# Kernel tuning notes

Measured on AMD Instinct MI355X. Metric: run time of the kernel, lower is better.

The kernel has to match this reference:

```python
import jax, jax.numpy as jnp
import numpy as np
from jax import lax

K_SIZE = 3
STRIDE = 1
PADDING = 1


def setup_inputs() -> dict:
    key = jax.random.key(0)
    k1, k2, k3 = jax.random.split(key, 3)
    x = jax.random.normal(k1, (4, 64, 64, 256), dtype=jnp.float32)
    # small offsets so bilinear sampling stays near the regular grid (realistic DCN behavior)
    offset_w = jax.random.normal(k2, (3, 3, 256, 27), dtype=jnp.float32) * 0.01
    offset_b = jnp.zeros((1, 1, 1, 27), dtype=jnp.float32)
    dcn_weight = jax.random.normal(k3, (256, 256, 3, 3), dtype=jnp.float32) * 0.02
    return {"x": x, "offset_w": offset_w, "offset_b": offset_b, "dcn_weight": dcn_weight}


def _dcnv2(x, offset_w, offset_b, dcn_weight):
    k, stride, padding = K_SIZE, STRIDE, PADDING
    N, H, W, C = x.shape
    kk = k * k
    # offset/mask prediction conv (stride=1 -> SAME padding, per original code)
    om = lax.conv_general_dilated(
        x, offset_w, window_strides=(stride, stride), padding='SAME',
        dimension_numbers=('NHWC', 'HWIO', 'NHWC')) + offset_b
    offset = om[..., : 2 * kk]                      # [N,oH,oW,2k^2] (y,x) pairs
    mask = jax.nn.sigmoid(om[..., 2 * kk:])         # [N,oH,oW,k^2]
    oH = (H + 2 * padding - (k - 1)) // stride
    oW = (W + 2 * padding - (k - 1)) // stride
    # asymmetric zero padding ((p, p+1), (p, p+1)) as in the original
    pad_x = jnp.pad(x, ((0, 0), (padding, padding + 1), (padding, padding + 1), (0, 0)))
    # sampling grid: base center + fixed kernel offsets + learned offsets
    base_y = jnp.arange(oH, dtype=x.dtype) * stride + padding   # [oH]
    base_x = jnp.arange(oW, dtype=x.dtype) * stride + padding   # [oW]
    kr = jnp.arange(k, dtype=x.dtype) - (k - 1) / 2.0
    inner_y = jnp.repeat(kr, k)   # [k^2], row-major (kH, kW)
    inner_x = jnp.tile(kr, k)
    off_yx = offset.reshape(N, oH, oW, kk, 2)
    pos_y = base_y[None, :, None, None] + inner_y[None, None, None, :] + off_yx[..., 0]
    pos_x = base_x[None, None, :, None] + inner_x[None, None, None, :] + off_yx[..., 1]
    pos_y = jnp.clip(pos_y, 0.0, H + 2 * padding - 1.0)
    pos_x = jnp.clip(pos_x, 0.0, W + 2 * padding - 1.0)
    y1 = jnp.floor(pos_y)
    x1 = jnp.floor(pos_x)
    y1i = y1.astype(jnp.int32)
    x1i = x1.astype(jnp.int32)
    y2i = y1i + 1
    x2i = x1i + 1
    gather = jax.vmap(lambda px, yi, xi: px[yi, xi])  # per-sample [oH,oW,k^2] -> [oH,oW,k^2,C]
    v1 = gather(pad_x, y1i, x1i)
    v2 = gather(pad_x, y1i, x2i)
    v3 = gather(pad_x, y2i, x1i)
    v4 = gather(pad_x, y2i, x2i)
    lh = (pos_y - y1)[..., None]
    lw = (pos_x - x1)[..., None]
    hh = 1.0 - lh
    hw = 1.0 - lw
    value = (hh * hw * v1 + hh * lw * v2 + lh * hw * v3 + lh * lw * v4) * mask[..., None]
    # [N,oH,oW,k^2,C] -> [N,oH,oW,C,k^2] -> [N,oH,oW,C*k^2], matching original layout
    value = jnp.transpose(value, (0, 1, 2, 4, 3)).reshape(N, oH, oW, C * kk)
    w = jnp.transpose(dcn_weight, (1, 2, 3, 0)).reshape(C * kk, -1)  # [C*k^2, out_C]
    return jnp.einsum('nhwc,cf->nhwf', value, w)


def reference(x, offset_w, offset_b, dcn_weight):
    return _dcnv2(x, offset_w, offset_b, dcn_weight)
```

## Files before the change

kernel.cpp:

```cpp
#include <hip/hip_runtime.h>
#include <hip/hip_fp16.h>
#include <math.h>

typedef __attribute__((ext_vector_type(8))) _Float16 f16x8;
typedef __attribute__((ext_vector_type(4))) float f32x4;

#define XP_OFF   0
#define XP_BYTES (4*67*67*256*2)
#define WT_OFF   XP_BYTES
#define WT_BYTES (2304*256*2)
#define WOT_OFF  (WT_OFF + WT_BYTES)
#define WOT_BYTES (2304*32*2)
#define OM_OFF   (WOT_OFF + WOT_BYTES)
#define OM_BYTES (16384*32*4)
#define V_OFF    (OM_OFF + OM_BYTES)
#define V_BYTES  ((size_t)16384*2304*2)
#define WS_NEED  ((size_t)V_OFF + V_BYTES)

#define AS1(p) ((const __attribute__((address_space(1))) void*)(p))
#define AS3(p) ((__attribute__((address_space(3))) void*)(p))

__global__ __launch_bounds__(256) void prep_all(const float* __restrict__ x,
        const float* __restrict__ dw, const float* __restrict__ ow,
        __half* __restrict__ xp, __half* __restrict__ wt, __half* __restrict__ wot) {
    int b = blockIdx.x, tid = threadIdx.x;
    if (b < 2245) {
        int g = b * 256 + tid;
        if (g >= 17956 * 32) return;
        int row = g >> 5, sub = g & 31;
        int n = row / 4489, rem = row - n * 4489;
        int yy = rem / 67,  xx = rem - yy * 67;
        __half* dst = xp + (size_t)row * 256 + sub * 8;
        union { uint4 u; __half2 h[4]; } r;
        r.u = make_uint4(0u, 0u, 0u, 0u);
        if (yy >= 1 && yy <= 64 && xx >= 1 && xx <= 64) {
            const float* src = x + (((size_t)n * 64 + (yy - 1)) * 64 + (xx - 1)) * 256 + sub * 8;
            float4 a = *(const float4*)src;
            float4 c = *(const float4*)(src + 4);
            r.h[0] = __float22half2_rn(make_float2(a.x, a.y));
            r.h[1] = __float22half2_rn(make_float2(a.z, a.w));
            r.h[2] = __float22half2_rn(make_float2(c.x, c.y));
            r.h[3] = __float22half2_rn(make_float2(c.z, c.w));
        }
        *(uint4*)dst = r.u;
    } else if (b < 2501) {
        int oc = b - 2245, c = tid;
        const float* src = dw + oc * 2304 + c * 9;
        __half* dst = wt + oc * 2304 + c;
        #pragma unroll
        for (int t = 0; t < 9; ++t) dst[t * 256] = __float2half(src[t]);
    } else {
        int g = (b - 2501) * 256 + tid;
        int oc = g & 31, idx = g >> 5;
        float v = (oc < 27) ? ow[idx * 27 + oc] : 0.f;
        wot[oc * 2304 + idx] = __float2half(v);
    }
}

__global__ __launch_bounds__(256) void offset_mfma4(const __half* __restrict__ xp,
        const __half* __restrict__ wot, const float* __restrict__ ob,
        float* __restrict__ om) {
    __shared__ __align__(16) char sA[2][16384];
    int tid = threadIdx.x, lane = tid & 63, wave = tid >> 6;
    int bid = blockIdx.x;
    int mt = (bid & 7) * 64 + (bid >> 3);
    int p0 = mt * 32;
    int n = p0 >> 12, y = (p0 & 4095) >> 6, w0 = p0 & 63;
    const char* xpn = (const char*)(xp + (size_t)n * 4489 * 256);
    int wr = wave >> 1, wc = wave & 1;
    int ar = lane & 15, kl = (lane >> 4) * 8;

    int soff[4];
    #pragma unroll
    for (int q = 0; q < 4; ++q) {
        int d = (q * 256 + tid) * 16;
        int row = d >> 9;
        soff[q] = row * 512 + ((d & 511) ^ ((row & 7) << 4));
    }

    f32x4 acc = {0.f, 0.f, 0.f, 0.f};
    int r_a = wr * 16 + ar;
    int rsw = (r_a & 7) << 4;
    const __half* bb = wot + (size_t)(wc * 16 + ar) * 2304 + kl;

    #pragma unroll
    for (int q = 0; q < 4; ++q)
        __builtin_amdgcn_global_load_lds(AS1(xpn + ((y * 67 + w0) << 9) + soff[q]),
                                         AS3(&sA[0][(q * 256 + tid) * 16]), 16, 0, 0);
    __syncthreads();

    for (int t = 0; t < 9; ++t) {
        int buf = t & 1;
        if (t < 8) {
            int t1 = t + 1;
            int ty = t1 / 3, tx = t1 - 3 * ty;
            int sb = ((y + ty) * 67 + w0 + tx) << 9;
            #pragma unroll
            for (int q = 0; q < 4; ++q)
                __builtin_amdgcn_global_load_lds(AS1(xpn + sb + soff[q]),
                                                 AS3(&sA[buf ^ 1][(q * 256 + tid) * 16]), 16, 0, 0);
        }
        const __half* bp = bb + t * 256;
        #pragma unroll
        for (int c0 = 0; c0 < 256; c0 += 32) {
            f16x8 a = *(const f16x8*)(&sA[buf][0] + r_a * 512 + (((c0 + kl) * 2) ^ rsw));
            f16x8 b = *(const f16x8*)(bp + c0);
            acc = __builtin_amdgcn_mfma_f32_16x16x32_f16(a, b, acc, 0, 0, 0);
        }
        __syncthreads();
    }

    int col = wc * 16 + ar;
    float bias = (col < 27) ? ob[col] : 0.f;
    int rj = (lane >> 4) * 4;
    #pragma unroll
    for (int j = 0; j < 4; ++j)
        om[(size_t)(p0 + wr * 16 + rj + j) * 32 + col] = acc[j] + bias;
}

__global__ __launch_bounds__(256) void sample_v(const __half* __restrict__ xp,
        const float* __restrict__ om, __half* __restrict__ V) {
    int g = blockIdx.x * 256 + threadIdx.x;
    int j = g >> 5;
    int s = g & 31;
    int p = j / 9;
    int t = j - p * 9;
    int n = p >> 12, y = (p >> 6) & 63, w = p & 63;
    const float* omp = om + (size_t)p * 32;
    float offy = omp[2 * t];
    float offx = omp[2 * t + 1];
    float mraw = omp[18 + t];
    float mask = 1.f / (1.f + __expf(-mraw));
    float py = (float)(y + 1) + (float)(t / 3 - 1) + offy;
    float px = (float)(w + 1) + (float)(t % 3 - 1) + offx;
    py = fminf(fmaxf(py, 0.f), 65.f);
    px = fminf(fmaxf(px, 0.f), 65.f);
    float y1f = floorf(py), x1f = floorf(px);
    int y1 = (int)y1f, x1 = (int)x1f;
    float ly = py - y1f, lx = px - x1f, hy = 1.f - ly, hx = 1.f - lx;
    const __half* b = xp + (size_t)n * 4489 * 256 + ((y1 * 67 + x1) << 8) + s * 8;
    union { uint4 u; __half2 h[4]; } cA, cB, cC, cD, r;
    cA.u = *(const uint4*)(b);
    cB.u = *(const uint4*)(b + 256);
    cC.u = *(const uint4*)(b + 17152);
    cD.u = *(const uint4*)(b + 17408);
    __half2 W11 = __float2half2_rn(hy * hx * mask), W12 = __float2half2_rn(hy * lx * mask);
    __half2 W21 = __float2half2_rn(ly * hx * mask), W22 = __float2half2_rn(ly * lx * mask);
    #pragma unroll
    for (int i = 0; i < 4; ++i)
        r.h[i] = __hfma2(cD.h[i], W22, __hfma2(cC.h[i], W21,
                 __hfma2(cB.h[i], W12, __hmul2(cA.h[i], W11))));
    *(uint4*)((char*)V + (size_t)g * 16) = r.u;
}

__global__ __launch_bounds__(256) void gemm_v2(const __half* __restrict__ V,
        const __half* __restrict__ wt, float* __restrict__ out) {
    __shared__ __align__(16) char sA[2][8192];
    __shared__ __align__(16) char sB[2][16384];
    int tid = threadIdx.x, lane = tid & 63, wave = tid >> 6;
    int bid = blockIdx.x;
    int xcd = bid & 7, idx = bid >> 3;
    int mt = xcd * 32 + (idx >> 1);
    int nt = idx & 1;
    int p0 = mt * 64, oc0 = nt * 128;
    int wr = wave >> 1, wc = wave & 1;
    int ar = lane & 15, kl = (lane >> 4) * 8;

    const char* aS[2]; const char* bS[4];
    #pragma unroll
    for (int q = 0; q < 2; ++q) {
        int d = (q * 256 + tid) * 16;
        int row = d >> 7, wb = d & 127;
        aS[q] = (const char*)V + (size_t)(p0 + row) * 4608 + (wb ^ ((row & 7) << 4));
    }
    #pragma unroll
    for (int q = 0; q < 4; ++q) {
        int d = (q * 256 + tid) * 16;
        int row = d >> 7, wb = d & 127;
        bS[q] = (const char*)wt + (size_t)(oc0 + row) * 4608 + (wb ^ ((row & 7) << 4));
    }

    f32x4 acc[2][4];
    #pragma unroll
    for (int m = 0; m < 2; ++m)
        #pragma unroll
        for (int nn = 0; nn < 4; ++nn) acc[m][nn] = (f32x4){0.f,0.f,0.f,0.f};

    #pragma unroll
    for (int q = 0; q < 2; ++q)
        __builtin_amdgcn_global_load_lds(AS1(aS[q]), AS3(&sA[0][(q * 256 + tid) * 16]), 16, 0, 0);
    #pragma unroll
    for (int q = 0; q < 4; ++q)
        __builtin_amdgcn_global_load_lds(AS1(bS[q]), AS3(&sB[0][(q * 256 + tid) * 16]), 16, 0, 0);
    __syncthreads();

    for (int kt = 0; kt < 36; ++kt) {
        int buf = kt & 1;
        if (kt < 35) {
            int kb = (kt + 1) * 128;
            #pragma unroll
            for (int q = 0; q < 2; ++q)
                __builtin_amdgcn_global_load_lds(AS1(aS[q] + kb), AS3(&sA[buf ^ 1][(q * 256 + tid) * 16]), 16, 0, 0);
            #pragma unroll
            for (int q = 0; q < 4; ++q)
                __builtin_amdgcn_global_load_lds(AS1(bS[q] + kb), AS3(&sB[buf ^ 1][(q * 256 + tid) * 16]), 16, 0, 0);
        }
        #pragma unroll
        for (int kk = 0; kk < 2; ++kk) {
            int ko = kk * 64 + kl * 2;
            f16x8 af[2], bf[4];
            #pragma unroll
            for (int m = 0; m < 2; ++m) {
                int r = wr * 32 + m * 16 + ar;
                af[m] = *(const f16x8*)(&sA[buf][0] + r * 128 + (ko ^ ((r & 7) << 4)));
            }
            #pragma unroll
            for (int nn = 0; nn < 4; ++nn) {
                int r = wc * 64 + nn * 16 + ar;
                bf[nn] = *(const f16x8*)(&sB[buf][0] + r * 128 + (ko ^ ((r & 7) << 4)));
            }
            #pragma unroll
            for (int m = 0; m < 2; ++m)
                #pragma unroll
                for (int nn = 0; nn < 4; ++nn)
                    acc[m][nn] = __builtin_amdgcn_mfma_f32_16x16x32_f16(af[m], bf[nn], acc[m][nn], 0, 0, 0);
        }
        __syncthreads();
    }

    int rj = (lane >> 4) * 4;
    #pragma unroll
    for (int m = 0; m < 2; ++m)
        #pragma unroll
        for (int nn = 0; nn < 4; ++nn)
            #pragma unroll
            for (int j = 0; j < 4; ++j)
                out[(size_t)(p0 + wr * 32 + m * 16 + rj + j) * 256 + oc0 + wc * 64 + nn * 16 + ar] = acc[m][nn][j];
}

__global__ __launch_bounds__(512) void dcn_mfma3(const __half* __restrict__ xp,
        const float* __restrict__ om, const __half* __restrict__ wt,
        float* __restrict__ out) {
    __shared__ char  s_v[16 * 512];
    __shared__ float s_ly[16][9], s_lx[16][9], s_m[16][9];
    __shared__ int   s_y1[16][9], s_x1[16][9];
    int tid  = threadIdx.x;
    int lane = tid & 63;
    int wave = tid >> 6;
    int bid  = blockIdx.x;
    int swzb = (bid & 7) * 128 + (bid >> 3);
    int p0 = swzb * 16;
    int n  = p0 >> 12;
    int y  = (p0 & 4095) >> 6;
    int w0 = p0 & 63;
    const __half* xpn = xp + (size_t)n * 4489 * 256;
    if (tid < 144) {
        int ps = tid / 9, k = tid - 9 * ps;
        int p  = p0 + ps;
        float offy = om[(size_t)p * 32 + 2 * k];
        float offx = om[(size_t)p * 32 + 2 * k + 1];
        float mraw = om[(size_t)p * 32 + 18 + k];
        float mask = 1.f / (1.f + __expf(-mraw));
        float py = (float)(y + 1)       + (float)(k / 3 - 1) + offy;
        float px = (float)(w0 + ps + 1) + (float)(k % 3 - 1) + offx;
        py = fminf(fmaxf(py, 0.f), 65.f);
        px = fminf(fmaxf(px, 0.f), 65.f);
        float y1f = floorf(py), x1f = floorf(px);
        s_y1[ps][k] = (int)y1f;
        s_x1[ps][k] = (int)x1f;
        s_ly[ps][k] = py - y1f;
        s_lx[ps][k] = px - x1f;
        s_m [ps][k] = mask;
    }
    __syncthreads();
    int px = tid >> 5;
    int ch = (tid & 31) * 8;
    int ar = lane & 15;
    int kl = (lane >> 4) * 8;
    int oc0 = wave * 32;
    const __half* bp0 = wt + (size_t)(oc0 + ar) * 2304 + kl;
    const __half* bp1 = wt + (size_t)(oc0 + 16 + ar) * 2304 + kl;
    int wr_off = px * 512 + (((tid & 31) * 16) ^ ((px & 7) << 4));
    int rd_row = ar * 512;
    int rd_swz = (ar & 7) << 4;
    f32x4 acc0 = {0.f,0.f,0.f,0.f}, acc1 = {0.f,0.f,0.f,0.f};
    for (int t = 0; t < 9; ++t) {
        int y1 = s_y1[px][t], x1 = s_x1[px][t];
        const __half* b = xpn + ((size_t)(y1 * 67 + x1) << 8) + ch;
        union { uint4 u; __half2 h[4]; } cA, cB, cC, cD, r;
        cA.u = *(const uint4*)(b);
        cB.u = *(const uint4*)(b + 256);
        cC.u = *(const uint4*)(b + 17152);
        cD.u = *(const uint4*)(b + 17408);
        float ly = s_ly[px][t], lx = s_lx[px][t], mk = s_m[px][t];
        float hy = 1.f - ly, hx = 1.f - lx;
        __half2 W11 = __float2half2_rn(hy * hx * mk);
        __half2 W12 = __float2half2_rn(hy * lx * mk);
        __half2 W21 = __float2half2_rn(ly * hx * mk);
        __half2 W22 = __float2half2_rn(ly * lx * mk);
        #pragma unroll
        for (int i = 0; i < 4; ++i)
            r.h[i] = __hfma2(cD.h[i], W22, __hfma2(cC.h[i], W21,
                     __hfma2(cB.h[i], W12, __hmul2(cA.h[i], W11))));
        *(uint4*)(s_v + wr_off) = r.u;
        __syncthreads();
        const __half* b0 = bp0 + t * 256;
        const __half* b1 = bp1 + t * 256;
        #pragma unroll
        for (int c0 = 0; c0 < 256; c0 += 32) {
            f16x8 a   = *(const f16x8*)(s_v + rd_row + (((c0 + kl) * 2) ^ rd_swz));
            f16x8 vb0 = *(const f16x8*)(b0 + c0);
            f16x8 vb1 = *(const f16x8*)(b1 + c0);
            acc0 = __builtin_amdgcn_mfma_f32_16x16x32_f16(a, vb0, acc0, 0, 0, 0);
            acc1 = __builtin_amdgcn_mfma_f32_16x16x32_f16(a, vb1, acc1, 0, 0, 0);
        }
        __syncthreads();
    }
    int rj = (lane >> 4) * 4;
    #pragma unroll
    for (int j = 0; j < 4; ++j) {
        out[(size_t)(p0 + rj + j) * 256 + oc0 + ar]      = acc0[j];
        out[(size_t)(p0 + rj + j) * 256 + oc0 + 16 + ar] = acc1[j];
    }
}

extern "C" void kernel_launch(void* const* d_in, const int* in_sizes, int n_in,
                              void* d_out, int out_size, void* d_ws, size_t ws_size,
                              hipStream_t stream) {
    const float* x  = (const float*)d_in[0];
    const float* ow = (const float*)d_in[1];
    const float* ob = (const float*)d_in[2];
    const float* dw = (const float*)d_in[3];
    __half* xpp = (__half*)((char*)d_ws + XP_OFF);
    __half* wt  = (__half*)((char*)d_ws + WT_OFF);
    __half* wot = (__half*)((char*)d_ws + WOT_OFF);
    float*  omp = (float*)((char*)d_ws + OM_OFF);
    __half* Vp  = (__half*)((char*)d_ws + V_OFF);
    float* out = (float*)d_out;

    hipLaunchKernelGGL(prep_all,     dim3(2789), dim3(256), 0, stream, x, dw, ow, xpp, wt, wot);
    hipLaunchKernelGGL(offset_mfma4, dim3(512),  dim3(256), 0, stream, xpp, wot, ob, omp);
    if (ws_size >= WS_NEED) {
        hipLaunchKernelGGL(sample_v, dim3(18432), dim3(256), 0, stream, xpp, omp, Vp);
        hipLaunchKernelGGL(gemm_v2,  dim3(512),   dim3(256), 0, stream, Vp, wt, out);
    } else {
        hipLaunchKernelGGL(dcn_mfma3, dim3(1024), dim3(512), 0, stream, xpp, omp, wt, out);
    }
}
```

Before: 85.11 us.

## Load GEMM B operand from pre-swizzled fragment layout directly into registers

Adds a prep pass that writes the deformable-conv weights in an MFMA-fragment-ordered layout, so the new GEMM kernel loads B fragments straight from global memory into registers instead of staging them through LDS. The GEMM now uses 128-thread blocks where each wave computes a 64x64 tile, with only A double-buffered in LDS and the k-loop manually unrolled by two. The sampling kernel also gets an XCD-aware block remap. This cuts LDS traffic and LDS size per block, in exchange for more registers per thread, fewer waves per block, and reliance on cache hits for the repeated B fragment loads.

```diff
diff --git a/kernel.cpp b/kernel.cpp
--- a/kernel.cpp
+++ b/kernel.cpp
@@ -9,7 +9,9 @@
 #define XP_BYTES (4*67*67*256*2)
 #define WT_OFF   XP_BYTES
 #define WT_BYTES (2304*256*2)
-#define WOT_OFF  (WT_OFF + WT_BYTES)
+#define WTF_OFF  (WT_OFF + WT_BYTES)
+#define WTF_BYTES (2304*256*2)
+#define WOT_OFF  (WTF_OFF + WTF_BYTES)
 #define WOT_BYTES (2304*32*2)
 #define OM_OFF   (WOT_OFF + WOT_BYTES)
 #define OM_BYTES (16384*32*4)
@@ -22,7 +24,8 @@
 
 __global__ __launch_bounds__(256) void prep_all(const float* __restrict__ x,
         const float* __restrict__ dw, const float* __restrict__ ow,
-        __half* __restrict__ xp, __half* __restrict__ wt, __half* __restrict__ wot) {
+        __half* __restrict__ xp, __half* __restrict__ wt, __half* __restrict__ wtf,
+        __half* __restrict__ wot) {
     int b = blockIdx.x, tid = threadIdx.x;
     if (b < 2245) {
         int g = b * 256 + tid;
@@ -49,8 +52,21 @@
         __half* dst = wt + oc * 2304 + c;
         #pragma unroll
         for (int t = 0; t < 9; ++t) dst[t * 256] = __float2half(src[t]);
+    } else if (b < 2789) {
+        int g = (b - 2501) * 256 + tid;
+        int l = g & 63, G = g >> 6;
+        int kg = G % 72, ocg = G / 72;
+        int oc = ocg * 16 + (l & 15);
+        int k  = kg * 32 + ((l >> 4) << 3);
+        int t  = k >> 8, c = k & 255;
+        const float* src = dw + (size_t)oc * 2304 + c * 9 + t;
+        union { uint4 u; __half2 h[4]; } r;
+        #pragma unroll
+        for (int j = 0; j < 4; ++j)
+            r.h[j] = __floats2half2_rn(src[(2 * j) * 9], src[(2 * j + 1) * 9]);
+        *(uint4*)(wtf + (size_t)g * 8) = r.u;
     } else {
-        int g = (b - 2501) * 256 + tid;
+        int g = (b - 2789) * 256 + tid;
         int oc = g & 31, idx = g >> 5;
         float v = (oc < 27) ? ow[idx * 27 + oc] : 0.f;
         wot[oc * 2304 + idx] = __float2half(v);
@@ -104,8 +120,8 @@
         #pragma unroll
         for (int c0 = 0; c0 < 256; c0 += 32) {
             f16x8 a = *(const f16x8*)(&sA[buf][0] + r_a * 512 + (((c0 + kl) * 2) ^ rsw));
-            f16x8 b = *(const f16x8*)(bp + c0);
-            acc = __builtin_amdgcn_mfma_f32_16x16x32_f16(a, b, acc, 0, 0, 0);
+            f16x8 bfr = *(const f16x8*)(bp + c0);
+            acc = __builtin_amdgcn_mfma_f32_16x16x32_f16(a, bfr, acc, 0, 0, 0);
         }
         __syncthreads();
     }
@@ -120,7 +136,9 @@
 
 __global__ __launch_bounds__(256) void sample_v(const __half* __restrict__ xp,
         const float* __restrict__ om, __half* __restrict__ V) {
-    int g = blockIdx.x * 256 + threadIdx.x;
+    int bid = blockIdx.x;
+    int gb  = (bid & 7) * 2304 + (bid >> 3);
+    int g = gb * 256 + threadIdx.x;
     int j = g >> 5;
     int s = g & 31;
     int p = j / 9;
@@ -153,89 +171,88 @@
     *(uint4*)((char*)V + (size_t)g * 16) = r.u;
 }
 
-__global__ __launch_bounds__(256) void gemm_v2(const __half* __restrict__ V,
-        const __half* __restrict__ wt, float* __restrict__ out) {
+#define STAGE_A(DST, KT) do { \
+    _Pragma("unroll") \
+    for (int q = 0; q < 4; ++q) \
+        __builtin_amdgcn_global_load_lds(AS1(aS[q] + (size_t)(KT) * 128), \
+                                         AS3((DST) + (q * 128 + tid) * 16), 16, 0, 0); \
+} while (0)
+
+#define LOAD_B(D0, D1, KT) do { \
+    _Pragma("unroll") \
+    for (int nn = 0; nn < 4; ++nn) { \
+        D0[nn] = *(const f16x8*)(bbase + ((size_t)nn * 72 + (KT) * 2 + 0) * 512); \
+        D1[nn] = *(const f16x8*)(bbase + ((size_t)nn * 72 + (KT) * 2 + 1) * 512); \
+    } \
+} while (0)
+
+#define STEP_K(SBUF, BARR, KK) do { \
+    _Pragma("unroll") \
+    for (int m = 0; m < 4; ++m) { \
+        int r_ = m * 16 + ar; \
+        f16x8 af_ = *(const f16x8*)((SBUF) + r_ * 128 + (((KK) * 64 + kl * 2) ^ ((r_ & 7) << 4))); \
+        _Pragma("unroll") \
+        for (int nn = 0; nn < 4; ++nn) \
+            acc[m][nn] = __builtin_amdgcn_mfma_f32_16x16x32_f16(af_, (BARR)[nn], acc[m][nn], 0, 0, 0); \
+    } \
+} while (0)
+
+__global__ __launch_bounds__(128) void gemm_v3(const __half* __restrict__ V,
+        const __half* __restrict__ wtf, float* __restrict__ out) {
     __shared__ __align__(16) char sA[2][8192];
-    __shared__ __align__(16) char sB[2][16384];
-    int tid = threadIdx.x, lane = tid & 63, wave = tid >> 6;
+    int tid = threadIdx.x, lane = tid & 63, wv = tid >> 6;
     int bid = blockIdx.x;
     int xcd = bid & 7, idx = bid >> 3;
     int mt = xcd * 32 + (idx >> 1);
     int nt = idx & 1;
-    int p0 = mt * 64, oc0 = nt * 128;
-    int wr = wave >> 1, wc = wave & 1;
+    int p0 = mt * 64;
     int ar = lane & 15, kl = (lane >> 4) * 8;
 
-    const char* aS[2]; const char* bS[4];
-    #pragma unroll
-    for (int q = 0; q < 2; ++q) {
-        int d = (q * 256 + tid) * 16;
+    const char* aS[4];
+    #pragma unroll
+    for (int q = 0; q < 4; ++q) {
+        int d = (q * 128 + tid) * 16;
         int row = d >> 7, wb = d & 127;
         aS[q] = (const char*)V + (size_t)(p0 + row) * 4608 + (wb ^ ((row & 7) << 4));
     }
-    #pragma unroll
-    for (int q = 0; q < 4; ++q) {
-        int d = (q * 256 + tid) * 16;
-        int row = d >> 7, wb = d & 127;
-        bS[q] = (const char*)wt + (size_t)(oc0 + row) * 4608 + (wb ^ ((row & 7) << 4));
-    }
-
-    f32x4 acc[2][4];
-    #pragma unroll
-    for (int m = 0; m < 2; ++m)
-        #pragma unroll
-        for (int nn = 0; nn < 4; ++nn) acc[m][nn] = (f32x4){0.f,0.f,0.f,0.f};
-
-    #pragma unroll
-    for (int q = 0; q < 2; ++q)
-        __builtin_amdgcn_global_load_lds(AS1(aS[q]), AS3(&sA[0][(q * 256 + tid) * 16]), 16, 0, 0);
-    #pragma unroll
-    for (int q = 0; q < 4; ++q)
-        __builtin_amdgcn_global_load_lds(AS1(bS[q]), AS3(&sB[0][(q * 256 + tid) * 16]), 16, 0, 0);
+    const __half* bbase = wtf + ((size_t)(nt * 8 + wv * 4) * 72 * 64 + lane) * 8;
+
+    f32x4 acc[4][4];
+    #pragma unroll
+    for (int m = 0; m < 4; ++m)
+        #pragma unroll
+        for (int nn = 0; nn < 4; ++nn) acc[m][nn] = (f32x4){0.f, 0.f, 0.f, 0.f};
+
+    f16x8 b0_0[4], b0_1[4], b1_0[4], b1_1[4];
+
+    LOAD_B(b0_0, b0_1, 0);
+    STAGE_A(&sA[0][0], 0);
     __syncthreads();
 
-    for (int kt = 0; kt < 36; ++kt) {
-        int buf = kt & 1;
-        if (kt < 35) {
-            int kb = (kt + 1) * 128;
-            #pragma unroll
-            for (int q = 0; q < 2; ++q)
-                __builtin_amdgcn_global_load_lds(AS1(aS[q] + kb), AS3(&sA[buf ^ 1][(q * 256 + tid) * 16]), 16, 0, 0);
-            #pragma unroll
-            for (int q = 0; q < 4; ++q)
-                __builtin_amdgcn_global_load_lds(AS1(bS[q] + kb), AS3(&sB[buf ^ 1][(q * 256 + tid) * 16]), 16, 0, 0);
-        }
-        #pragma unroll
-        for (int kk = 0; kk < 2; ++kk) {
-            int ko = kk * 64 + kl * 2;
-            f16x8 af[2], bf[4];
-            #pragma unroll
-            for (int m = 0; m < 2; ++m) {
-                int r = wr * 32 + m * 16 + ar;
-                af[m] = *(const f16x8*)(&sA[buf][0] + r * 128 + (ko ^ ((r & 7) << 4)));
-            }
-            #pragma unroll
-            for (int nn = 0; nn < 4; ++nn) {
-                int r = wc * 64 + nn * 16 + ar;
-                bf[nn] = *(const f16x8*)(&sB[buf][0] + r * 128 + (ko ^ ((r & 7) << 4)));
-            }
-            #pragma unroll
-            for (int m = 0; m < 2; ++m)
-                #pragma unroll
-                for (int nn = 0; nn < 4; ++nn)
-                    acc[m][nn] = __builtin_amdgcn_mfma_f32_16x16x32_f16(af[m], bf[nn], acc[m][nn], 0, 0, 0);
-        }
+    for (int kt = 0; kt < 36; kt += 2) {
+        STAGE_A(&sA[1][0], kt + 1);
+        LOAD_B(b1_0, b1_1, kt + 1);
+        STEP_K(&sA[0][0], b0_0, 0);
+        STEP_K(&sA[0][0], b0_1, 1);
+        __syncthreads();
+        if (kt + 2 < 36) {
+            STAGE_A(&sA[0][0], kt + 2);
+            LOAD_B(b0_0, b0_1, kt + 2);
+        }
+        STEP_K(&sA[1][0], b1_0, 0);
+        STEP_K(&sA[1][0], b1_1, 1);
         __syncthreads();
     }
 
     int rj = (lane >> 4) * 4;
-    #pragma unroll
-    for (int m = 0; m < 2; ++m)
+    int ocb = nt * 128 + wv * 64;
+    #pragma unroll
+    for (int m = 0; m < 4; ++m)
         #pragma unroll
         for (int nn = 0; nn < 4; ++nn)
             #pragma unroll
             for (int j = 0; j < 4; ++j)
-                out[(size_t)(p0 + wr * 32 + m * 16 + rj + j) * 256 + oc0 + wc * 64 + nn * 16 + ar] = acc[m][nn][j];
+                out[(size_t)(p0 + m * 16 + rj + j) * 256 + ocb + nn * 16 + ar] = acc[m][nn][j];
 }
 
 __global__ __launch_bounds__(512) void dcn_mfma3(const __half* __restrict__ xp,
@@ -333,16 +350,17 @@
     const float* dw = (const float*)d_in[3];
     __half* xpp = (__half*)((char*)d_ws + XP_OFF);
     __half* wt  = (__half*)((char*)d_ws + WT_OFF);
+    __half* wtf = (__half*)((char*)d_ws + WTF_OFF);
     __half* wot = (__half*)((char*)d_ws + WOT_OFF);
     float*  omp = (float*)((char*)d_ws + OM_OFF);
     __half* Vp  = (__half*)((char*)d_ws + V_OFF);
     float* out = (float*)d_out;
 
-    hipLaunchKernelGGL(prep_all,     dim3(2789), dim3(256), 0, stream, x, dw, ow, xpp, wt, wot);
+    hipLaunchKernelGGL(prep_all,     dim3(3077), dim3(256), 0, stream, x, dw, ow, xpp, wt, wtf, wot);
     hipLaunchKernelGGL(offset_mfma4, dim3(512),  dim3(256), 0, stream, xpp, wot, ob, omp);
     if (ws_size >= WS_NEED) {
         hipLaunchKernelGGL(sample_v, dim3(18432), dim3(256), 0, stream, xpp, omp, Vp);
-        hipLaunchKernelGGL(gemm_v2,  dim3(512),   dim3(256), 0, stream, Vp, wt, out);
+        hipLaunchKernelGGL(gemm_v3,  dim3(512),   dim3(128), 0, stream, Vp, wtf, out);
     } else {
         hipLaunchKernelGGL(dcn_mfma3, dim3(1024), dim3(512), 0, stream, xpp, omp, wt, out);
     }
```

New measurement: 92.02 us. 1.08x slower.

## Split-K the sampled-value GEMM into two halves with a reduction pass

Applied to the files above, without the earlier changes.

The im2col GEMM is split along K into two halves, doubling the grid from 512 to 1024 blocks, so more CUs are busy on the 256-CU part. Partial fp32 results go to a new workspace buffer and a separate reduce kernel sums them into the output. The sampling kernel also gets an XCD-aware block remap to improve cache locality. The split adds 32 MB of partial-sum traffic, one extra kernel launch, and a larger workspace requirement, which could make the default path fall back to the fused kernel if the workspace is too small.

```diff
diff --git a/kernel.cpp b/kernel.cpp
--- a/kernel.cpp
+++ b/kernel.cpp
@@ -15,7 +15,9 @@
 #define OM_BYTES (16384*32*4)
 #define V_OFF    (OM_OFF + OM_BYTES)
 #define V_BYTES  ((size_t)16384*2304*2)
-#define WS_NEED  ((size_t)V_OFF + V_BYTES)
+#define P_OFF    (V_OFF + V_BYTES)
+#define P_BYTES  ((size_t)2*16384*256*4)
+#define WS_NEED  ((size_t)P_OFF + P_BYTES)
 
 #define AS1(p) ((const __attribute__((address_space(1))) void*)(p))
 #define AS3(p) ((__attribute__((address_space(3))) void*)(p))
@@ -104,8 +106,8 @@
         #pragma unroll
         for (int c0 = 0; c0 < 256; c0 += 32) {
             f16x8 a = *(const f16x8*)(&sA[buf][0] + r_a * 512 + (((c0 + kl) * 2) ^ rsw));
-            f16x8 b = *(const f16x8*)(bp + c0);
-            acc = __builtin_amdgcn_mfma_f32_16x16x32_f16(a, b, acc, 0, 0, 0);
+            f16x8 bfr = *(const f16x8*)(bp + c0);
+            acc = __builtin_amdgcn_mfma_f32_16x16x32_f16(a, bfr, acc, 0, 0, 0);
         }
         __syncthreads();
     }
@@ -120,7 +122,9 @@
 
 __global__ __launch_bounds__(256) void sample_v(const __half* __restrict__ xp,
         const float* __restrict__ om, __half* __restrict__ V) {
-    int g = blockIdx.x * 256 + threadIdx.x;
+    int bid = blockIdx.x;
+    int gb  = (bid & 7) * 2304 + (bid >> 3);
+    int g = gb * 256 + threadIdx.x;
     int j = g >> 5;
     int s = g & 31;
     int p = j / 9;
@@ -153,31 +157,33 @@
     *(uint4*)((char*)V + (size_t)g * 16) = r.u;
 }
 
-__global__ __launch_bounds__(256) void gemm_v2(const __half* __restrict__ V,
-        const __half* __restrict__ wt, float* __restrict__ out) {
+__global__ __launch_bounds__(256) void gemm_ks(const __half* __restrict__ V,
+        const __half* __restrict__ wt, float* __restrict__ P) {
     __shared__ __align__(16) char sA[2][8192];
     __shared__ __align__(16) char sB[2][16384];
     int tid = threadIdx.x, lane = tid & 63, wave = tid >> 6;
     int bid = blockIdx.x;
     int xcd = bid & 7, idx = bid >> 3;
-    int mt = xcd * 32 + (idx >> 1);
-    int nt = idx & 1;
+    int mt = xcd * 32 + (idx >> 2);
+    int nt = (idx >> 1) & 1;
+    int ks = idx & 1;
     int p0 = mt * 64, oc0 = nt * 128;
     int wr = wave >> 1, wc = wave & 1;
     int ar = lane & 15, kl = (lane >> 4) * 8;
+    size_t ksb = (size_t)ks * 2304;
 
     const char* aS[2]; const char* bS[4];
     #pragma unroll
     for (int q = 0; q < 2; ++q) {
         int d = (q * 256 + tid) * 16;
         int row = d >> 7, wb = d & 127;
-        aS[q] = (const char*)V + (size_t)(p0 + row) * 4608 + (wb ^ ((row & 7) << 4));
+        aS[q] = (const char*)V + (size_t)(p0 + row) * 4608 + ksb + (wb ^ ((row & 7) << 4));
     }
     #pragma unroll
     for (int q = 0; q < 4; ++q) {
         int d = (q * 256 + tid) * 16;
         int row = d >> 7, wb = d & 127;
-        bS[q] = (const char*)wt + (size_t)(oc0 + row) * 4608 + (wb ^ ((row & 7) << 4));
+        bS[q] = (const char*)wt + (size_t)(oc0 + row) * 4608 + ksb + (wb ^ ((row & 7) << 4));
     }
 
     f32x4 acc[2][4];
@@ -194,9 +200,9 @@
         __builtin_amdgcn_global_load_lds(AS1(bS[q]), AS3(&sB[0][(q * 256 + tid) * 16]), 16, 0, 0);
     __syncthreads();
 
-    for (int kt = 0; kt < 36; ++kt) {
+    for (int kt = 0; kt < 18; ++kt) {
         int buf = kt & 1;
-        if (kt < 35) {
+        if (kt < 17) {
             int kb = (kt + 1) * 128;
             #pragma unroll
             for (int q = 0; q < 2; ++q)
@@ -228,6 +234,7 @@
         __syncthreads();
     }
 
+    float* Pk = P + (size_t)ks * 16384 * 256;
     int rj = (lane >> 4) * 4;
     #pragma unroll
     for (int m = 0; m < 2; ++m)
@@ -235,7 +242,21 @@
         for (int nn = 0; nn < 4; ++nn)
             #pragma unroll
             for (int j = 0; j < 4; ++j)
-                out[(size_t)(p0 + wr * 32 + m * 16 + rj + j) * 256 + oc0 + wc * 64 + nn * 16 + ar] = acc[m][nn][j];
+                Pk[(size_t)(p0 + wr * 32 + m * 16 + rj + j) * 256 + oc0 + wc * 64 + nn * 16 + ar] = acc[m][nn][j];
+}
+
+__global__ __launch_bounds__(256) void reduce_p(const float* __restrict__ P,
+        float* __restrict__ out) {
+    int g = blockIdx.x * 256 + threadIdx.x;
+    const float4* p0 = (const float4*)P;
+    const float4* p1 = (const float4*)(P + (size_t)16384 * 256);
+    float4* o = (float4*)out;
+    #pragma unroll
+    for (int i = 0; i < 4; ++i) {
+        int idx = g * 4 + i;
+        float4 a = p0[idx], b = p1[idx];
+        o[idx] = make_float4(a.x + b.x, a.y + b.y, a.z + b.z, a.w + b.w);
+    }
 }
 
 __global__ __launch_bounds__(512) void dcn_mfma3(const __half* __restrict__ xp,
@@ -336,13 +357,15 @@
     __half* wot = (__half*)((char*)d_ws + WOT_OFF);
     float*  omp = (float*)((char*)d_ws + OM_OFF);
     __half* Vp  = (__half*)((char*)d_ws + V_OFF);
+    float*  Pp  = (float*)((char*)d_ws + P_OFF);
     float* out = (float*)d_out;
 
     hipLaunchKernelGGL(prep_all,     dim3(2789), dim3(256), 0, stream, x, dw, ow, xpp, wt, wot);
     hipLaunchKernelGGL(offset_mfma4, dim3(512),  dim3(256), 0, stream, xpp, wot, ob, omp);
     if (ws_size >= WS_NEED) {
         hipLaunchKernelGGL(sample_v, dim3(18432), dim3(256), 0, stream, xpp, omp, Vp);
-        hipLaunchKernelGGL(gemm_v2,  dim3(512),   dim3(256), 0, stream, Vp, wt, out);
+        hipLaunchKernelGGL(gemm_ks,  dim3(1024),  dim3(256), 0, stream, Vp, wt, Pp);
+        hipLaunchKernelGGL(reduce_p, dim3(1024),  dim3(256), 0, stream, Pp, out);
     } else {
         hipLaunchKernelGGL(dcn_mfma3, dim3(1024), dim3(512), 0, stream, xpp, omp, wt, out);
     }
```

After: 96.87 us. 13.8% more time.

## Triple-buffer GEMM with vmcnt waits and remap sample_v blocks across XCDs

Applied to the files above, without the earlier changes.

The V-GEMM moves from a double-buffered LDS pipeline with a full __syncthreads per k-step to a three-stage ring. Explicit s_waitcnt vmcnt counts and raw barriers keep two tiles of global_load_lds in flight while the current one is computed, and s_setprio raises priority around the MFMA bursts. The sampling kernel remaps block IDs so consecutive work lands on the same XCD, which should improve L2 locality for the gathered input. The cost is 50% more LDS per block, which may reduce occupancy, and correctness now depends on the hand-tuned vmcnt values being right.

```diff
diff --git a/kernel.cpp b/kernel.cpp
--- a/kernel.cpp
+++ b/kernel.cpp
@@ -104,8 +104,8 @@
         #pragma unroll
         for (int c0 = 0; c0 < 256; c0 += 32) {
             f16x8 a = *(const f16x8*)(&sA[buf][0] + r_a * 512 + (((c0 + kl) * 2) ^ rsw));
-            f16x8 b = *(const f16x8*)(bp + c0);
-            acc = __builtin_amdgcn_mfma_f32_16x16x32_f16(a, b, acc, 0, 0, 0);
+            f16x8 bfr = *(const f16x8*)(bp + c0);
+            acc = __builtin_amdgcn_mfma_f32_16x16x32_f16(a, bfr, acc, 0, 0, 0);
         }
         __syncthreads();
     }
@@ -120,7 +120,9 @@
 
 __global__ __launch_bounds__(256) void sample_v(const __half* __restrict__ xp,
         const float* __restrict__ om, __half* __restrict__ V) {
-    int g = blockIdx.x * 256 + threadIdx.x;
+    int bid = blockIdx.x;
+    int gb  = (bid & 7) * 2304 + (bid >> 3);
+    int g = gb * 256 + threadIdx.x;
     int j = g >> 5;
     int s = g & 31;
     int p = j / 9;
@@ -153,10 +155,49 @@
     *(uint4*)((char*)V + (size_t)g * 16) = r.u;
 }
 
-__global__ __launch_bounds__(256) void gemm_v2(const __half* __restrict__ V,
+#define WAITVM(N) do { asm volatile("s_waitcnt vmcnt(" #N ")" ::: "memory"); \
+                       __builtin_amdgcn_sched_barrier(0); } while (0)
+
+#define STAGE_V4(BUF, KT) do { \
+    _Pragma("unroll") \
+    for (int q = 0; q < 2; ++q) \
+        __builtin_amdgcn_global_load_lds(AS1(aS[q] + (size_t)(KT) * 128), \
+            AS3(&sA[BUF][(q * 256 + tid) * 16]), 16, 0, 0); \
+    _Pragma("unroll") \
+    for (int q = 0; q < 4; ++q) \
+        __builtin_amdgcn_global_load_lds(AS1(bS[q] + (size_t)(KT) * 128), \
+            AS3(&sB[BUF][(q * 256 + tid) * 16]), 16, 0, 0); \
+} while (0)
+
+#define COMPUTE_V4(BUF) do { \
+    _Pragma("unroll") \
+    for (int kk = 0; kk < 2; ++kk) { \
+        int ko = kk * 64 + kl * 2; \
+        f16x8 af[2], bf[4]; \
+        _Pragma("unroll") \
+        for (int m = 0; m < 2; ++m) { \
+            int r = wr * 32 + m * 16 + ar; \
+            af[m] = *(const f16x8*)(&sA[BUF][0] + r * 128 + (ko ^ ((r & 7) << 4))); \
+        } \
+        _Pragma("unroll") \
+        for (int nn = 0; nn < 4; ++nn) { \
+            int r = wc * 64 + nn * 16 + ar; \
+            bf[nn] = *(const f16x8*)(&sB[BUF][0] + r * 128 + (ko ^ ((r & 7) << 4))); \
+        } \
+        __builtin_amdgcn_s_setprio(1); \
+        _Pragma("unroll") \
+        for (int m = 0; m < 2; ++m) \
+            _Pragma("unroll") \
+            for (int nn = 0; nn < 4; ++nn) \
+                acc[m][nn] = __builtin_amdgcn_mfma_f32_16x16x32_f16(af[m], bf[nn], acc[m][nn], 0, 0, 0); \
+        __builtin_amdgcn_s_setprio(0); \
+    } \
+} while (0)
+
+__global__ __launch_bounds__(256) void gemm_v4(const __half* __restrict__ V,
         const __half* __restrict__ wt, float* __restrict__ out) {
-    __shared__ __align__(16) char sA[2][8192];
-    __shared__ __align__(16) char sB[2][16384];
+    __shared__ __align__(16) char sA[3][8192];
+    __shared__ __align__(16) char sB[3][16384];
     int tid = threadIdx.x, lane = tid & 63, wave = tid >> 6;
     int bid = blockIdx.x;
     int xcd = bid & 7, idx = bid >> 3;
@@ -186,47 +227,28 @@
         #pragma unroll
         for (int nn = 0; nn < 4; ++nn) acc[m][nn] = (f32x4){0.f,0.f,0.f,0.f};
 
-    #pragma unroll
-    for (int q = 0; q < 2; ++q)
-        __builtin_amdgcn_global_load_lds(AS1(aS[q]), AS3(&sA[0][(q * 256 + tid) * 16]), 16, 0, 0);
-    #pragma unroll
-    for (int q = 0; q < 4; ++q)
-        __builtin_amdgcn_global_load_lds(AS1(bS[q]), AS3(&sB[0][(q * 256 + tid) * 16]), 16, 0, 0);
-    __syncthreads();
-
-    for (int kt = 0; kt < 36; ++kt) {
-        int buf = kt & 1;
-        if (kt < 35) {
-            int kb = (kt + 1) * 128;
-            #pragma unroll
-            for (int q = 0; q < 2; ++q)
-                __builtin_amdgcn_global_load_lds(AS1(aS[q] + kb), AS3(&sA[buf ^ 1][(q * 256 + tid) * 16]), 16, 0, 0);
-            #pragma unroll
-            for (int q = 0; q < 4; ++q)
-                __builtin_amdgcn_global_load_lds(AS1(bS[q] + kb), AS3(&sB[buf ^ 1][(q * 256 + tid) * 16]), 16, 0, 0);
-        }
-        #pragma unroll
-        for (int kk = 0; kk < 2; ++kk) {
-            int ko = kk * 64 + kl * 2;
-            f16x8 af[2], bf[4];
-            #pragma unroll
-            for (int m = 0; m < 2; ++m) {
-                int r = wr * 32 + m * 16 + ar;
-                af[m] = *(const f16x8*)(&sA[buf][0] + r * 128 + (ko ^ ((r & 7) << 4)));
-            }
-            #pragma unroll
-            for (int nn = 0; nn < 4; ++nn) {
-                int r = wc * 64 + nn * 16 + ar;
-                bf[nn] = *(const f16x8*)(&sB[buf][0] + r * 128 + (ko ^ ((r & 7) << 4)));
-            }
-            #pragma unroll
-            for (int m = 0; m < 2; ++m)
-                #pragma unroll
-                for (int nn = 0; nn < 4; ++nn)
-                    acc[m][nn] = __builtin_amdgcn_mfma_f32_16x16x32_f16(af[m], bf[nn], acc[m][nn], 0, 0, 0);
-        }
-        __syncthreads();
-    }
+    STAGE_V4(0, 0);
+    STAGE_V4(1, 1);
+    STAGE_V4(2, 2);
+
+    for (int kt = 0; kt < 34; ++kt) {
+        int buf = kt % 3;
+        WAITVM(12);
+        __builtin_amdgcn_s_barrier();
+        __builtin_amdgcn_sched_barrier(0);
+        COMPUTE_V4(buf);
+        __builtin_amdgcn_s_barrier();
+        STAGE_V4(buf, kt + 3);
+    }
+    WAITVM(6);
+    __builtin_amdgcn_s_barrier();
+    __builtin_amdgcn_sched_barrier(0);
+    COMPUTE_V4(34 % 3);
+    __builtin_amdgcn_s_barrier();
+    WAITVM(0);
+    __builtin_amdgcn_s_barrier();
+    __builtin_amdgcn_sched_barrier(0);
+    COMPUTE_V4(35 % 3);
 
     int rj = (lane >> 4) * 4;
     #pragma unroll
@@ -342,7 +364,7 @@
     hipLaunchKernelGGL(offset_mfma4, dim3(512),  dim3(256), 0, stream, xpp, wot, ob, omp);
     if (ws_size >= WS_NEED) {
         hipLaunchKernelGGL(sample_v, dim3(18432), dim3(256), 0, stream, xpp, omp, Vp);
-        hipLaunchKernelGGL(gemm_v2,  dim3(512),   dim3(256), 0, stream, Vp, wt, out);
+        hipLaunchKernelGGL(gemm_v4,  dim3(512),   dim3(256), 0, stream, Vp, wt, out);
     } else {
         hipLaunchKernelGGL(dcn_mfma3, dim3(1024), dim3(512), 0, stream, xpp, omp, wt, out);
     }
```

Result: faster. 81.33 us (-4.4%).
